# Optimization experiments

Measured on AMD Instinct MI355X. Metric: run time of the kernel, lower is better.

Reference implementation:

```python
import jax, jax.numpy as jnp
import numpy as np

DT = 0.1  # module buffer `dt`
I_DIM, H_DIM, BATCH, SEQ = 128, 64, 8, 4096


def setup_inputs() -> dict:
    key = jax.random.key(0)
    ks = jax.random.split(key, 6)
    return {
        "x": jax.random.normal(ks[0], (BATCH, SEQ, I_DIM), dtype=jnp.float32),
        "B": jax.random.uniform(ks[1], (I_DIM, H_DIM), dtype=jnp.float32),
        "C_tilde": jax.random.uniform(ks[2], (I_DIM, H_DIM), dtype=jnp.float32),
        "Lambda": jax.random.uniform(ks[3], (I_DIM, 1, H_DIM), dtype=jnp.float32),
        "P": jax.random.uniform(ks[4], (I_DIM, H_DIM), dtype=jnp.float32),
        "Q": jax.random.uniform(ks[5], (I_DIM, H_DIM), dtype=jnp.float32),
    }


def _compute_K(B, C_tilde, Lambda, P, Q, L):
    # omega_k = exp(2*pi*i*k/L), k = 0..L-1
    n = jnp.arange(L, dtype=jnp.float32)
    omega = jnp.exp((2j * jnp.pi / L) * n).astype(jnp.complex64)          # [L]
    g = (2.0 / DT) * ((1.0 - omega) / (1.0 + omega))                      # [L]
    # denominator: [I, L, H] complex (the big intermediate)
    inv = 1.0 / (g[None, :, None] - Lambda.astype(jnp.complex64))
    a0, a1 = jnp.conj(C_tilde), Q                                          # [I, H]
    b0, b1 = B, P                                                          # [I, H]
    # Cauchy dot products: sum over hidden dim -> [I, L]
    k00 = jnp.einsum('ih,ilh->il', (a0 * b0).astype(jnp.complex64), inv)
    k01 = jnp.einsum('ih,ilh->il', (a0 * b1).astype(jnp.complex64), inv)
    k10 = jnp.einsum('ih,ilh->il', (a1 * b0).astype(jnp.complex64), inv)
    k11 = jnp.einsum('ih,ilh->il', (a1 * b1).astype(jnp.complex64), inv)
    c = 2.0 / (1.0 + omega)                                                # [L]
    K_hat = c[None, :] * (k00 - k01 * (1.0 + k11) * k10)                   # [I, L]
    # irfft crops input along last axis to L//2 + 1 bins (matches torch)
    return jnp.fft.irfft(K_hat, n=L, axis=-1)                              # [I, L] real


def reference(x, B, C_tilde, Lambda, P, Q):
    Bz, L, I = x.shape
    K = _compute_K(B, C_tilde, Lambda, P, Q, L)        # [I, L]
    xt = jnp.transpose(x, (0, 2, 1))                   # [B, I, L]
    n2 = 2 * L
    x_fft = jnp.fft.rfft(xt, n=n2, axis=2)             # zero-pad to 2L -> [B, I, L+1]
    K_fft = jnp.fft.rfft(K, n=n2, axis=1)[None]        # [1, I, L+1]
    y = jnp.fft.irfft(x_fft * K_fft, n=n2, axis=2)[:, :, :L]
    return jnp.transpose(y, (0, 2, 1))                 # [B, L, I]
```

## Files before the change

kernel.cpp:

```cpp
#include <hip/hip_runtime.h>

#define I_DIM 128
#define H_DIM 64
#define BATCH 8
#define SEQ   4096
#define NBIN  (SEQ/2 + 1)
#define NBIN2 (SEQ + 1)

#define SZ(a) ((a) ^ (((a) >> 4) & 15))

__device__ float2 g_Kf[I_DIM * NBIN2];
__device__ float2 g_Xf[(size_t)BATCH * I_DIM * SEQ];

__device__ inline float2 cmul(float2 a, float2 b) {
    return make_float2(a.x * b.x - a.y * b.y, a.x * b.y + a.y * b.x);
}
__device__ inline float2 cadd(float2 a, float2 b) { return make_float2(a.x + b.x, a.y + b.y); }
__device__ inline float2 csub(float2 a, float2 b) { return make_float2(a.x - b.x, a.y - b.y); }

__device__ inline void dft8(float2 a[8]) {
    const float C = 0.70710678118654752f;
    float2 s0 = cadd(a[0], a[4]), s1 = cadd(a[1], a[5]);
    float2 s2 = cadd(a[2], a[6]), s3 = cadd(a[3], a[7]);
    float2 d0 = csub(a[0], a[4]), d1 = csub(a[1], a[5]);
    float2 d2 = csub(a[2], a[6]), d3 = csub(a[3], a[7]);
    d1 = make_float2(C * (d1.x + d1.y), C * (d1.y - d1.x));
    d2 = make_float2(d2.y, -d2.x);
    d3 = make_float2(C * (d3.y - d3.x), -C * (d3.x + d3.y));
    {
        float2 p0 = cadd(s0, s2), p1 = cadd(s1, s3);
        float2 m0 = csub(s0, s2), m1 = csub(s1, s3);
        m1 = make_float2(m1.y, -m1.x);
        a[0] = cadd(p0, p1); a[4] = csub(p0, p1);
        a[2] = cadd(m0, m1); a[6] = csub(m0, m1);
    }
    {
        float2 p0 = cadd(d0, d2), p1 = cadd(d1, d3);
        float2 m0 = csub(d0, d2), m1 = csub(d1, d3);
        m1 = make_float2(m1.y, -m1.x);
        a[1] = cadd(p0, p1); a[5] = csub(p0, p1);
        a[3] = cadd(m0, m1); a[7] = csub(m0, m1);
    }
}

__device__ inline void dft4(float2 a[4]) {
    float2 p0 = cadd(a[0], a[2]), p1 = cadd(a[1], a[3]);
    float2 m0 = csub(a[0], a[2]), m1 = csub(a[1], a[3]);
    m1 = make_float2(m1.y, -m1.x);
    a[0] = cadd(p0, p1); a[2] = csub(p0, p1);
    a[1] = cadd(m0, m1); a[3] = csub(m0, m1);
}

template <int N, int S, int NT>
__device__ inline void stage8(float2* __restrict__ lds, int tid) {
    constexpr int NB = N / 8;
    constexpr int ITER = (NB + NT - 1) / NT;
    const bool act = (NB >= NT) || (tid < NB);
    float2 d[ITER][8];
#pragma unroll
    for (int b = 0; b < ITER; ++b) {
        const int u = tid + b * NT;
        if (act) {
#pragma unroll
            for (int j = 0; j < 8; ++j)
                d[b][j] = lds[SZ(u + NB * j)];
        }
    }
    __syncthreads();
#pragma unroll
    for (int b = 0; b < ITER; ++b) {
        const int u = tid + b * NT;
        if (act) {
            const int q = u & (S - 1);
            dft8(d[b]);
            if constexpr (S < NB) {
                const float cang = (float)(-6.283185307179586) / (float)N;
                float sn, cs;
                __sincosf(cang * (float)(u - q), &sn, &cs);
                const float2 w = make_float2(cs, sn);
                float2 t = w;
#pragma unroll
                for (int k = 1; k < 8; ++k) {
                    d[b][k] = cmul(d[b][k], t);
                    if (k < 7) t = cmul(t, w);
                }
            }
            const int base = 8 * u - 7 * q;
#pragma unroll
            for (int k = 0; k < 8; ++k)
                lds[SZ(base + k * S)] = d[b][k];
        }
    }
    __syncthreads();
}

template <int N, int S, int NT>
__device__ inline void stage4(float2* __restrict__ lds, int tid) {
    constexpr int NB = N / 4;
    constexpr int ITER = (NB + NT - 1) / NT;
    const bool act = (NB >= NT) || (tid < NB);
    float2 d[ITER][4];
#pragma unroll
    for (int b = 0; b < ITER; ++b) {
        const int u = tid + b * NT;
        if (act) {
#pragma unroll
            for (int j = 0; j < 4; ++j)
                d[b][j] = lds[SZ(u + NB * j)];
        }
    }
    __syncthreads();
#pragma unroll
    for (int b = 0; b < ITER; ++b) {
        const int u = tid + b * NT;
        if (act) {
            const int q = u & (S - 1);
            dft4(d[b]);
            if constexpr (S < NB) {
                const float cang = (float)(-6.283185307179586) / (float)N;
                float sn, cs;
                __sincosf(cang * (float)(u - q), &sn, &cs);
                const float2 w = make_float2(cs, sn);
                float2 t = w;
#pragma unroll
                for (int k = 1; k < 4; ++k) {
                    d[b][k] = cmul(d[b][k], t);
                    if (k < 3) t = cmul(t, w);
                }
            }
            const int base = 4 * u - 3 * q;
#pragma unroll
            for (int k = 0; k < 4; ++k)
                lds[SZ(base + k * S)] = d[b][k];
        }
    }
    __syncthreads();
}

__device__ inline void stage8_first_halfzero(float2* __restrict__ lds, int tid) {
    const float C = 0.70710678118654752f;
    float2 a0 = lds[SZ(tid)];
    float2 a1 = lds[SZ(tid + 512)];
    float2 a2 = lds[SZ(tid + 1024)];
    float2 a3 = lds[SZ(tid + 1536)];
    __syncthreads();
    float2 p0 = cadd(a0, a2), p1 = cadd(a1, a3);
    float2 m0 = csub(a0, a2), m1t = csub(a1, a3);
    float2 m1 = make_float2(m1t.y, -m1t.x);
    float2 b0 = cadd(p0, p1), b4 = csub(p0, p1);
    float2 b2 = cadd(m0, m1), b6 = csub(m0, m1);
    float2 c1 = make_float2(C * (a1.x + a1.y), C * (a1.y - a1.x));
    float2 c2 = make_float2(a2.y, -a2.x);
    float2 c3 = make_float2(C * (a3.y - a3.x), -C * (a3.x + a3.y));
    float2 q0 = cadd(a0, c2), q1 = cadd(c1, c3);
    float2 n0 = csub(a0, c2), n1t = csub(c1, c3);
    float2 n1 = make_float2(n1t.y, -n1t.x);
    float2 b1 = cadd(q0, q1), b5 = csub(q0, q1);
    float2 b3 = cadd(n0, n1), b7 = csub(n0, n1);
    float sn, cs;
    __sincosf((float)(-6.283185307179586 / 4096.0) * (float)tid, &sn, &cs);
    float2 w1 = make_float2(cs, sn);
    float2 w2 = cmul(w1, w1), w3 = cmul(w2, w1), w4 = cmul(w2, w2);
    float2 w5 = cmul(w3, w2), w6 = cmul(w3, w3), w7 = cmul(w4, w3);
    const int base = 8 * tid;
    lds[SZ(base + 0)] = b0;
    lds[SZ(base + 1)] = cmul(b1, w1);
    lds[SZ(base + 2)] = cmul(b2, w2);
    lds[SZ(base + 3)] = cmul(b3, w3);
    lds[SZ(base + 4)] = cmul(b4, w4);
    lds[SZ(base + 5)] = cmul(b5, w5);
    lds[SZ(base + 6)] = cmul(b6, w6);
    lds[SZ(base + 7)] = cmul(b7, w7);
    __syncthreads();
}

__device__ inline void stage8_last_half(float2* __restrict__ lds, int tid) {
    float2 d[8];
#pragma unroll
    for (int j = 0; j < 8; ++j) d[j] = lds[SZ(tid + 512 * j)];
    __syncthreads();
    dft8(d);
#pragma unroll
    for (int k = 0; k < 4; ++k) lds[SZ(tid + 512 * k)] = d[k];
    __syncthreads();
}

__device__ inline void combine_pair(float2* __restrict__ lds,
                                    const float2* __restrict__ Kfrow,
                                    int m, bool write_partner) {
    float2 Zq = lds[SZ(m & 4095)];
    float2 Zr = lds[SZ((4096 - m) & 4095)];
    float sn, cs;
    __sincosf((float)(-3.141592653589793 / 4096.0) * (float)m, &sn, &cs);
    float pr = Zq.x + Zr.x, pi2 = Zq.y - Zr.y;
    float dr = Zq.x - Zr.x, di = Zq.y + Zr.y;
    float jt_r = -sn * dr - cs * di;
    float jt_i =  cs * dr - sn * di;
    float2 Xm  = make_float2(0.5f * (pr - jt_r),  0.5f * ( pi2 - jt_i));
    float2 Xm2 = make_float2(0.5f * (pr + jt_r),  0.5f * (-pi2 - jt_i));
    float2 Ym  = cmul(Xm,  Kfrow[m]);
    float2 Ym2 = cmul(Xm2, Kfrow[4096 - m]);
    float qr = Ym.x + Ym2.x, qi = Ym.y - Ym2.y;
    float er = Ym.x - Ym2.x, ei = Ym.y + Ym2.y;
    float gr2 = sn * er - cs * ei;
    float gi2 = sn * ei + cs * er;
    lds[SZ(m & 4095)] = make_float2(0.5f * (qr + gr2), -0.5f * (qi + gi2));
    if (write_partner)
        lds[SZ(4096 - m)] = make_float2(0.5f * (qr - gr2), 0.5f * (qi - gi2));
}

__global__ __launch_bounds__(512) void s4_stage1_kernel(const float* __restrict__ x,
                                                        const float* __restrict__ Bm,
                                                        const float* __restrict__ Cm,
                                                        const float* __restrict__ Lm,
                                                        const float* __restrict__ Pm,
                                                        const float* __restrict__ Qm) {
    __shared__ float2 lds[4096];
    const int tid = threadIdx.x;

    if (blockIdx.x < I_DIM) {
        const int i = blockIdx.x;
        {
            const float* Brow = Bm + i * H_DIM;
            const float* Crow = Cm + i * H_DIM;
            const float* Lrow = Lm + i * H_DIM;
            const float* Prow = Pm + i * H_DIM;
            const float* Qrow = Qm + i * H_DIM;
            for (int k = tid; k < NBIN; k += 512) {
                float theta = (float)(6.283185307179586 / (double)SEQ) * (float)k;
                float sn, cs;
                sincosf(theta, &sn, &cs);
                float tr = 1.0f - cs, ti = -sn;
                float br = 1.0f + cs, bi = sn;
                float idn = 1.0f / (br * br + bi * bi);
                float gr = 20.0f * (tr * br + ti * bi) * idn;
                float gi = 20.0f * (ti * br - tr * bi) * idn;
                float cr = 2.0f * br * idn;
                float ci = -2.0f * bi * idn;

                float k00r = 0.f, k00i = 0.f, k01r = 0.f, k01i = 0.f;
                float k10r = 0.f, k10i = 0.f, k11r = 0.f, k11i = 0.f;
#pragma unroll 8
                for (int h = 0; h < H_DIM; ++h) {
                    float lam = Lrow[h];
                    float drr = gr - lam;
                    float dii = gi;
                    float im = 1.0f / (drr * drr + dii * dii);
                    float ivr = drr * im;
                    float ivi = -dii * im;
                    float bv = Brow[h], cv = Crow[h], pv = Prow[h], qv = Qrow[h];
                    float cb = cv * bv;
                    float cp = cv * pv;
                    float qb = qv * bv;
                    float qp = qv * pv;
                    k00r += cb * ivr; k00i += cb * ivi;
                    k01r += cp * ivr; k01i += cp * ivi;
                    k10r += qb * ivr; k10i += qb * ivi;
                    k11r += qp * ivr; k11i += qp * ivi;
                }
                float t1r = 1.0f + k11r, t1i = k11i;
                float t2r = k01r * t1r - k01i * t1i;
                float t2i = k01r * t1i + k01i * t1r;
                float t3r = t2r * k10r - t2i * k10i;
                float t3i = t2r * k10i + t2i * k10r;
                float nr = k00r - t3r, ni = k00i - t3i;
                lds[k] = make_float2(cr * nr - ci * ni, cr * ni + ci * nr);
            }
        }
        __syncthreads();

        float2 hm[4], hc[4];
#pragma unroll
        for (int r = 0; r < 4; ++r) {
            int m = tid + (r << 9);
            hm[r] = lds[m];
            hc[r] = lds[2048 - m];
        }
        __syncthreads();
#pragma unroll
        for (int r = 0; r < 4; ++r) {
            int m = tid + (r << 9);
            float pr = hm[r].x + hc[r].x, pi2 = hm[r].y - hc[r].y;
            float dr = hm[r].x - hc[r].x, di = hm[r].y + hc[r].y;
            float sn, cs;
            __sincosf((float)(3.141592653589793 / 2048.0) * (float)m, &sn, &cs);
            float Or = 0.5f * (cs * dr - sn * di);
            float Oi = 0.5f * (sn * dr + cs * di);
            lds[SZ(m)] = make_float2(0.5f * pr - Oi, -(0.5f * pi2 + Or));
        }
        __syncthreads();

        stage4<2048, 1,   512>(lds, tid);
        stage8<2048, 4,   512>(lds, tid);
        stage8<2048, 32,  512>(lds, tid);
        stage8<2048, 256, 512>(lds, tid);

        const float s1 = 1.0f / 2048.0f;
#pragma unroll
        for (int r = 0; r < 4; ++r) {
            int n = tid + (r << 9);
            float2 o = lds[SZ(n)];
            lds[SZ(n)]        = make_float2(o.x * s1, -o.y * s1);
            lds[SZ(n + 2048)] = make_float2(0.f, 0.f);
        }
        __syncthreads();

        stage8<4096, 1,   512>(lds, tid);
        stage8<4096, 8,   512>(lds, tid);
        stage8<4096, 64,  512>(lds, tid);
        stage8<4096, 512, 512>(lds, tid);

        float2* Kfrow = g_Kf + (size_t)i * NBIN2;
#pragma unroll
        for (int r = 0; r < 9; ++r) {
            int m = tid + (r << 9);
            if (m <= 4096) {
                float2 Zq = lds[SZ(m & 4095)];
                float2 Zr = lds[SZ((4096 - m) & 4095)];
                float sn, cs;
                __sincosf((float)(-3.141592653589793 / 4096.0) * (float)m, &sn, &cs);
                float pr = Zq.x + Zr.x, pi2 = Zq.y - Zr.y;
                float dr = Zq.x - Zr.x, di = Zq.y + Zr.y;
                float jt_r = -sn * dr - cs * di;
                float jt_i =  cs * dr - sn * di;
                Kfrow[m] = make_float2(0.5f * (pr - jt_r), 0.5f * (pi2 - jt_i));
            }
        }
    } else {
        const int blk = blockIdx.x - I_DIM;
        const int b = blk & 7;
        const int i = blk >> 3;

        const float* xb = x + (size_t)b * SEQ * I_DIM + i;
#pragma unroll
        for (int r = 0; r < 4; ++r) {
            int n = tid + (r << 9);
            float re = xb[(size_t)(2 * n) * I_DIM];
            float im = xb[(size_t)(2 * n + 1) * I_DIM];
            lds[SZ(n)] = make_float2(re, im);
        }
        __syncthreads();

        stage8_first_halfzero(lds, tid);
        stage8<4096, 8,   512>(lds, tid);
        stage8<4096, 64,  512>(lds, tid);
        stage8<4096, 512, 512>(lds, tid);

        float2* dst = g_Xf + (size_t)blk * SEQ;
#pragma unroll
        for (int r = 0; r < 8; ++r) {
            int n = tid + (r << 9);
            dst[n] = lds[SZ(n)];
        }
    }
}

__global__ __launch_bounds__(512) void s4_stage2_kernel(float* __restrict__ y) {
    __shared__ float2 lds[4096];
    const int tid = threadIdx.x;
    const int blk = blockIdx.x;
    const int b = blk & 7;
    const int i = blk >> 3;

    const float2* src = g_Xf + (size_t)blk * SEQ;
#pragma unroll
    for (int r = 0; r < 8; ++r) {
        int n = tid + (r << 9);
        lds[SZ(n)] = src[n];
    }
    __syncthreads();

    const float2* Kfrow = g_Kf + (size_t)i * NBIN2;
#pragma unroll
    for (int r = 0; r < 4; ++r) {
        int m = tid + (r << 9);
        combine_pair(lds, Kfrow, m, m != 0);
    }
    if (tid == 0)
        combine_pair(lds, Kfrow, 2048, false);
    __syncthreads();

    stage8<4096, 1,  512>(lds, tid);
    stage8<4096, 8,  512>(lds, tid);
    stage8<4096, 64, 512>(lds, tid);
    stage8_last_half(lds, tid);

    const float inv = 1.0f / 4096.0f;
    float* yb = y + (size_t)b * SEQ * I_DIM + i;
#pragma unroll
    for (int r = 0; r < 4; ++r) {
        int n = tid + (r << 9);
        float2 v = lds[SZ(n)];
        yb[(size_t)(2 * n) * I_DIM]     = v.x * inv;
        yb[(size_t)(2 * n + 1) * I_DIM] = -v.y * inv;
    }
}

extern "C" void kernel_launch(void* const* d_in, const int* in_sizes, int n_in,
                              void* d_out, int out_size, void* d_ws, size_t ws_size,
                              hipStream_t stream) {
    const float* x  = (const float*)d_in[0];
    const float* Bm = (const float*)d_in[1];
    const float* Cm = (const float*)d_in[2];
    const float* Lm = (const float*)d_in[3];
    const float* Pm = (const float*)d_in[4];
    const float* Qm = (const float*)d_in[5];
    float* out = (float*)d_out;

    s4_stage1_kernel<<<I_DIM + BATCH * I_DIM, 512, 0, stream>>>(x, Bm, Cm, Lm, Pm, Qm);
    s4_stage2_kernel<<<BATCH * I_DIM, 512, 0, stream>>>(out);
}
```

Measured before the change: 77.35 us.

## Fuse first and last FFT stages with global load/store to skip LDS round trips

Each FFT now performs its first radix stage directly on values loaded from global memory in registers, and its last radix stage directly before the global store. This drops the staging writes to shared memory and the matching barriers. In stage2, the real-FFT combine with the kernel spectrum is folded into the first butterfly, reading Xf and Kf straight from global memory. In exchange, register pressure rises and global reads in the combine step become scattered (indices m and 4096-m).

```diff
diff --git a/kernel.cpp b/kernel.cpp
--- a/kernel.cpp
+++ b/kernel.cpp
@@ -94,55 +94,10 @@
     __syncthreads();
 }
 
-template <int N, int S, int NT>
-__device__ inline void stage4(float2* __restrict__ lds, int tid) {
-    constexpr int NB = N / 4;
-    constexpr int ITER = (NB + NT - 1) / NT;
-    const bool act = (NB >= NT) || (tid < NB);
-    float2 d[ITER][4];
-#pragma unroll
-    for (int b = 0; b < ITER; ++b) {
-        const int u = tid + b * NT;
-        if (act) {
-#pragma unroll
-            for (int j = 0; j < 4; ++j)
-                d[b][j] = lds[SZ(u + NB * j)];
-        }
-    }
-    __syncthreads();
-#pragma unroll
-    for (int b = 0; b < ITER; ++b) {
-        const int u = tid + b * NT;
-        if (act) {
-            const int q = u & (S - 1);
-            dft4(d[b]);
-            if constexpr (S < NB) {
-                const float cang = (float)(-6.283185307179586) / (float)N;
-                float sn, cs;
-                __sincosf(cang * (float)(u - q), &sn, &cs);
-                const float2 w = make_float2(cs, sn);
-                float2 t = w;
-#pragma unroll
-                for (int k = 1; k < 4; ++k) {
-                    d[b][k] = cmul(d[b][k], t);
-                    if (k < 3) t = cmul(t, w);
-                }
-            }
-            const int base = 4 * u - 3 * q;
-#pragma unroll
-            for (int k = 0; k < 4; ++k)
-                lds[SZ(base + k * S)] = d[b][k];
-        }
-    }
-    __syncthreads();
-}
-
-__device__ inline void stage8_first_halfzero(float2* __restrict__ lds, int tid) {
+__device__ inline void halfzero4096_writeback(float2* __restrict__ lds, int tid,
+                                              float2 a0, float2 a1,
+                                              float2 a2, float2 a3) {
     const float C = 0.70710678118654752f;
-    float2 a0 = lds[SZ(tid)];
-    float2 a1 = lds[SZ(tid + 512)];
-    float2 a2 = lds[SZ(tid + 1024)];
-    float2 a3 = lds[SZ(tid + 1536)];
     __syncthreads();
     float2 p0 = cadd(a0, a2), p1 = cadd(a1, a3);
     float2 m0 = csub(a0, a2), m1t = csub(a1, a3);
@@ -174,41 +129,6 @@
     __syncthreads();
 }
 
-__device__ inline void stage8_last_half(float2* __restrict__ lds, int tid) {
-    float2 d[8];
-#pragma unroll
-    for (int j = 0; j < 8; ++j) d[j] = lds[SZ(tid + 512 * j)];
-    __syncthreads();
-    dft8(d);
-#pragma unroll
-    for (int k = 0; k < 4; ++k) lds[SZ(tid + 512 * k)] = d[k];
-    __syncthreads();
-}
-
-__device__ inline void combine_pair(float2* __restrict__ lds,
-                                    const float2* __restrict__ Kfrow,
-                                    int m, bool write_partner) {
-    float2 Zq = lds[SZ(m & 4095)];
-    float2 Zr = lds[SZ((4096 - m) & 4095)];
-    float sn, cs;
-    __sincosf((float)(-3.141592653589793 / 4096.0) * (float)m, &sn, &cs);
-    float pr = Zq.x + Zr.x, pi2 = Zq.y - Zr.y;
-    float dr = Zq.x - Zr.x, di = Zq.y + Zr.y;
-    float jt_r = -sn * dr - cs * di;
-    float jt_i =  cs * dr - sn * di;
-    float2 Xm  = make_float2(0.5f * (pr - jt_r),  0.5f * ( pi2 - jt_i));
-    float2 Xm2 = make_float2(0.5f * (pr + jt_r),  0.5f * (-pi2 - jt_i));
-    float2 Ym  = cmul(Xm,  Kfrow[m]);
-    float2 Ym2 = cmul(Xm2, Kfrow[4096 - m]);
-    float qr = Ym.x + Ym2.x, qi = Ym.y - Ym2.y;
-    float er = Ym.x - Ym2.x, ei = Ym.y + Ym2.y;
-    float gr2 = sn * er - cs * ei;
-    float gi2 = sn * ei + cs * er;
-    lds[SZ(m & 4095)] = make_float2(0.5f * (qr + gr2), -0.5f * (qi + gi2));
-    if (write_partner)
-        lds[SZ(4096 - m)] = make_float2(0.5f * (qr - gr2), 0.5f * (qi - gi2));
-}
-
 __global__ __launch_bounds__(512) void s4_stage1_kernel(const float* __restrict__ x,
                                                         const float* __restrict__ Bm,
                                                         const float* __restrict__ Cm,
@@ -269,43 +189,52 @@
         }
         __syncthreads();
 
-        float2 hm[4], hc[4];
-#pragma unroll
-        for (int r = 0; r < 4; ++r) {
-            int m = tid + (r << 9);
-            hm[r] = lds[m];
-            hc[r] = lds[2048 - m];
-        }
-        __syncthreads();
-#pragma unroll
-        for (int r = 0; r < 4; ++r) {
-            int m = tid + (r << 9);
-            float pr = hm[r].x + hc[r].x, pi2 = hm[r].y - hc[r].y;
-            float dr = hm[r].x - hc[r].x, di = hm[r].y + hc[r].y;
+        {
+            float2 z[4];
+#pragma unroll
+            for (int j = 0; j < 4; ++j) {
+                int m = tid + (j << 9);
+                float2 Hm = lds[m];
+                float2 Hc = lds[2048 - m];
+                float pr = Hm.x + Hc.x, pi2 = Hm.y - Hc.y;
+                float dr = Hm.x - Hc.x, di = Hm.y + Hc.y;
+                float sn, cs;
+                __sincosf((float)(3.141592653589793 / 2048.0) * (float)m, &sn, &cs);
+                float Or = 0.5f * (cs * dr - sn * di);
+                float Oi = 0.5f * (sn * dr + cs * di);
+                z[j] = make_float2(0.5f * pr - Oi, -(0.5f * pi2 + Or));
+            }
+            __syncthreads();
+            dft4(z);
             float sn, cs;
-            __sincosf((float)(3.141592653589793 / 2048.0) * (float)m, &sn, &cs);
-            float Or = 0.5f * (cs * dr - sn * di);
-            float Oi = 0.5f * (sn * dr + cs * di);
-            lds[SZ(m)] = make_float2(0.5f * pr - Oi, -(0.5f * pi2 + Or));
-        }
-        __syncthreads();
-
-        stage4<2048, 1,   512>(lds, tid);
+            __sincosf((float)(-6.283185307179586 / 2048.0) * (float)tid, &sn, &cs);
+            float2 w1 = make_float2(cs, sn);
+            float2 w2 = cmul(w1, w1);
+            float2 w3 = cmul(w2, w1);
+            z[1] = cmul(z[1], w1);
+            z[2] = cmul(z[2], w2);
+            z[3] = cmul(z[3], w3);
+            const int base = 4 * tid;
+#pragma unroll
+            for (int k = 0; k < 4; ++k) lds[SZ(base + k)] = z[k];
+            __syncthreads();
+        }
+
         stage8<2048, 4,   512>(lds, tid);
         stage8<2048, 32,  512>(lds, tid);
         stage8<2048, 256, 512>(lds, tid);
 
-        const float s1 = 1.0f / 2048.0f;
-#pragma unroll
-        for (int r = 0; r < 4; ++r) {
-            int n = tid + (r << 9);
-            float2 o = lds[SZ(n)];
-            lds[SZ(n)]        = make_float2(o.x * s1, -o.y * s1);
-            lds[SZ(n + 2048)] = make_float2(0.f, 0.f);
-        }
-        __syncthreads();
-
-        stage8<4096, 1,   512>(lds, tid);
+        {
+            const float s1 = 1.0f / 2048.0f;
+            float2 a[4];
+#pragma unroll
+            for (int j = 0; j < 4; ++j) {
+                float2 o = lds[SZ(tid + (j << 9))];
+                a[j] = make_float2(o.x * s1, -o.y * s1);
+            }
+            halfzero4096_writeback(lds, tid, a[0], a[1], a[2], a[3]);
+        }
+
         stage8<4096, 8,   512>(lds, tid);
         stage8<4096, 64,  512>(lds, tid);
         stage8<4096, 512, 512>(lds, tid);
@@ -332,26 +261,26 @@
         const int i = blk >> 3;
 
         const float* xb = x + (size_t)b * SEQ * I_DIM + i;
-#pragma unroll
-        for (int r = 0; r < 4; ++r) {
-            int n = tid + (r << 9);
-            float re = xb[(size_t)(2 * n) * I_DIM];
-            float im = xb[(size_t)(2 * n + 1) * I_DIM];
-            lds[SZ(n)] = make_float2(re, im);
-        }
-        __syncthreads();
-
-        stage8_first_halfzero(lds, tid);
-        stage8<4096, 8,   512>(lds, tid);
-        stage8<4096, 64,  512>(lds, tid);
-        stage8<4096, 512, 512>(lds, tid);
-
+        float2 a[4];
+#pragma unroll
+        for (int j = 0; j < 4; ++j) {
+            int n = tid + (j << 9);
+            a[j] = make_float2(xb[(size_t)(2 * n) * I_DIM],
+                               xb[(size_t)(2 * n + 1) * I_DIM]);
+        }
+        halfzero4096_writeback(lds, tid, a[0], a[1], a[2], a[3]);
+
+        stage8<4096, 8,  512>(lds, tid);
+        stage8<4096, 64, 512>(lds, tid);
+
+        float2 e[8];
+#pragma unroll
+        for (int j = 0; j < 8; ++j) e[j] = lds[SZ(tid + (j << 9))];
+        dft8(e);
         float2* dst = g_Xf + (size_t)blk * SEQ;
 #pragma unroll
-        for (int r = 0; r < 8; ++r) {
-            int n = tid + (r << 9);
-            dst[n] = lds[SZ(n)];
-        }
+        for (int k = 0; k < 8; ++k)
+            dst[tid + (k << 9)] = e[k];
     }
 }
 
@@ -361,38 +290,65 @@
     const int blk = blockIdx.x;
     const int b = blk & 7;
     const int i = blk >> 3;
-
-    const float2* src = g_Xf + (size_t)blk * SEQ;
-#pragma unroll
-    for (int r = 0; r < 8; ++r) {
-        int n = tid + (r << 9);
-        lds[SZ(n)] = src[n];
-    }
-    __syncthreads();
-
+    const float2* Xf = g_Xf + (size_t)blk * SEQ;
     const float2* Kfrow = g_Kf + (size_t)i * NBIN2;
-#pragma unroll
-    for (int r = 0; r < 4; ++r) {
-        int m = tid + (r << 9);
-        combine_pair(lds, Kfrow, m, m != 0);
-    }
-    if (tid == 0)
-        combine_pair(lds, Kfrow, 2048, false);
-    __syncthreads();
-
-    stage8<4096, 1,  512>(lds, tid);
+
+    float2 d[8];
+#pragma unroll
+    for (int j = 0; j < 8; ++j) {
+        int m = tid + (j << 9);
+        int mm = (4096 - m) & 4095;
+        float2 Zq = Xf[m];
+        float2 Zr = Xf[mm];
+        float2 Km  = Kfrow[m];
+        float2 Km2 = Kfrow[4096 - m];
+        float sn, cs;
+        __sincosf((float)(-3.141592653589793 / 4096.0) * (float)m, &sn, &cs);
+        float pr = Zq.x + Zr.x, pi2 = Zq.y - Zr.y;
+        float dr = Zq.x - Zr.x, di = Zq.y + Zr.y;
+        float jt_r = -sn * dr - cs * di;
+        float jt_i =  cs * dr - sn * di;
+        float2 Xm  = make_float2(0.5f * (pr - jt_r),  0.5f * ( pi2 - jt_i));
+        float2 Xm2 = make_float2(0.5f * (pr + jt_r),  0.5f * (-pi2 - jt_i));
+        float2 Ym  = cmul(Xm,  Km);
+        float2 Ym2 = cmul(Xm2, Km2);
+        float qr = Ym.x + Ym2.x, qi = Ym.y - Ym2.y;
+        float er = Ym.x - Ym2.x, ei = Ym.y + Ym2.y;
+        float gr2 = sn * er - cs * ei;
+        float gi2 = sn * ei + cs * er;
+        d[j] = make_float2(0.5f * (qr + gr2), -0.5f * (qi + gi2));
+    }
+
+    dft8(d);
+    {
+        float sn, cs;
+        __sincosf((float)(-6.283185307179586 / 4096.0) * (float)tid, &sn, &cs);
+        float2 w1 = make_float2(cs, sn);
+        float2 w2 = cmul(w1, w1), w3 = cmul(w2, w1), w4 = cmul(w2, w2);
+        float2 w5 = cmul(w3, w2), w6 = cmul(w3, w3), w7 = cmul(w4, w3);
+        d[1] = cmul(d[1], w1); d[2] = cmul(d[2], w2); d[3] = cmul(d[3], w3);
+        d[4] = cmul(d[4], w4); d[5] = cmul(d[5], w5); d[6] = cmul(d[6], w6);
+        d[7] = cmul(d[7], w7);
+    }
+    const int base = 8 * tid;
+#pragma unroll
+    for (int k = 0; k < 8; ++k) lds[SZ(base + k)] = d[k];
+    __syncthreads();
+
     stage8<4096, 8,  512>(lds, tid);
     stage8<4096, 64, 512>(lds, tid);
-    stage8_last_half(lds, tid);
-
+
+    float2 e[8];
+#pragma unroll
+    for (int j = 0; j < 8; ++j) e[j] = lds[SZ(tid + (j << 9))];
+    dft8(e);
     const float inv = 1.0f / 4096.0f;
     float* yb = y + (size_t)b * SEQ * I_DIM + i;
 #pragma unroll
-    for (int r = 0; r < 4; ++r) {
-        int n = tid + (r << 9);
-        float2 v = lds[SZ(n)];
-        yb[(size_t)(2 * n) * I_DIM]     = v.x * inv;
-        yb[(size_t)(2 * n + 1) * I_DIM] = -v.y * inv;
+    for (int k = 0; k < 4; ++k) {
+        int n = tid + (k << 9);
+        yb[(size_t)(2 * n) * I_DIM]     = e[k].x * inv;
+        yb[(size_t)(2 * n + 1) * I_DIM] = -e[k].y * inv;
     }
 }
 
```

New measurement: 78.50 us. No clear change (+1.5%).
